# Kernel optimization log

Hardware: AMD Instinct MI355X
Metric: run time of the kernel (lower is better)

Reference implementation:

```python
import jax, jax.numpy as jnp
import numpy as np

LOG2 = np.float32(np.log(2.0))

def _jsd_pos(p):
    # get_positive_expectation, measure='JSD', average=False
    return LOG2 - jax.nn.softplus(-p)

def setup_inputs() -> dict:
    key = jax.random.key(0)
    k1, k2, k3, k4, k5, k6 = jax.random.split(key, 6)
    N, G, D = 65536, 512, 256
    batch_1 = jnp.sort(jax.random.randint(k1, (N,), 0, G))
    batch_2 = jnp.sort(jax.random.randint(k2, (N,), 0, G))
    z1 = jax.random.normal(k3, (N, D), dtype=jnp.float32)
    z2 = jax.random.normal(k4, (N, D), dtype=jnp.float32)
    g1 = jax.random.normal(k5, (G, D), dtype=jnp.float32)
    g2 = jax.random.normal(k6, (G, D), dtype=jnp.float32)
    return {"batch_1": batch_1, "batch_2": batch_2, "z1": z1, "z2": z2, "g1": g1, "g2": g2}

def reference(batch_1, batch_2, z1, z2, g1, g2):
    # pos_mask scatter-build -> dense one-hot [N, G]
    pos_mask_1 = jax.nn.one_hot(batch_1, g1.shape[0], dtype=z1.dtype)
    pos_mask_2 = jax.nn.one_hot(batch_2, g2.shape[0], dtype=z2.dtype)
    # masked node-graph similarity matrices [N, G]
    self_sim_1 = (z1 @ g1.T) * pos_mask_1
    self_sim_2 = (z2 @ g2.T) * pos_mask_2
    cross_sim_12 = (z1 @ g2.T) * pos_mask_1
    cross_sim_21 = (z2 @ g1.T) * pos_mask_2
    # sep=True branch: per-node row sums, L2 distance over nodes
    self_js_11 = _jsd_pos(self_sim_1).sum(1)
    cross_js_12 = _jsd_pos(cross_sim_12).sum(1)
    self_js_22 = _jsd_pos(self_sim_2).sum(1)
    cross_js_21 = _jsd_pos(cross_sim_21).sum(1)
    L_1 = jnp.sqrt(jnp.sum((self_js_11 - cross_js_12) ** 2))
    L_2 = jnp.sqrt(jnp.sum((self_js_22 - cross_js_21) ** 2))
    return L_1 + L_2
```

## Files before the change

### kernel.cpp

```cpp
#include <hip/hip_runtime.h>
#include <math.h>

__device__ __forceinline__ float spn(float p) {
    return fmaxf(-p, 0.0f) + __logf(1.0f + __expf(-fabsf(p)));
}

__device__ __forceinline__ float dot4(float4 a, float4 b) {
    return a.x * b.x + a.y * b.y + a.z * b.z + a.w * b.w;
}

__device__ __forceinline__ float wave64_reduce(float x) {
    int t;
    t = __builtin_amdgcn_update_dpp(0, __builtin_bit_cast(int, x), 0x111, 0xf, 0xf, true);
    x += __builtin_bit_cast(float, t);
    t = __builtin_amdgcn_update_dpp(0, __builtin_bit_cast(int, x), 0x112, 0xf, 0xf, true);
    x += __builtin_bit_cast(float, t);
    t = __builtin_amdgcn_update_dpp(0, __builtin_bit_cast(int, x), 0x114, 0xf, 0xf, true);
    x += __builtin_bit_cast(float, t);
    t = __builtin_amdgcn_update_dpp(0, __builtin_bit_cast(int, x), 0x118, 0xf, 0xf, true);
    x += __builtin_bit_cast(float, t);
    t = __builtin_amdgcn_update_dpp(0, __builtin_bit_cast(int, x), 0x142, 0xa, 0xf, true);
    x += __builtin_bit_cast(float, t);
    t = __builtin_amdgcn_update_dpp(0, __builtin_bit_cast(int, x), 0x143, 0xc, 0xf, true);
    x += __builtin_bit_cast(float, t);
    return x;
}

typedef const void __attribute__((address_space(1)))* gas_ptr;
typedef void       __attribute__((address_space(3)))* las_ptr;

__device__ __forceinline__ void stage_row(const float* grow, float* lrow, int lane) {
    __builtin_amdgcn_global_load_lds((gas_ptr)(grow + lane * 4), (las_ptr)lrow,
                                     16, 0, 0);
}

#define NBLOCKS 4096
#define NPB 16
#define NPW 4

__global__ __launch_bounds__(256) void jsd_dot_kernel(
    const int*   __restrict__ b1,
    const int*   __restrict__ b2,
    const float* __restrict__ z1,
    const float* __restrict__ z2,
    const float* __restrict__ g1,
    const float* __restrict__ g2,
    float*       __restrict__ partials)
{
    __shared__ float zs1[NPB * 256];
    __shared__ float zs2[NPB * 256];

    const int wave = threadIdx.x >> 6;
    const int lane = threadIdx.x & 63;

    const int sbase = __builtin_amdgcn_readfirstlane(blockIdx.x * NPB + wave * NPW);

    #pragma unroll
    for (int j = 0; j < NPW; ++j) {
        stage_row(z1 + (size_t)(sbase + j) * 256, &zs1[(wave * NPW + j) * 256], lane);
        stage_row(z2 + (size_t)(sbase + j) * 256, &zs2[(wave * NPW + j) * 256], lane);
    }

    int i1[NPW], i2[NPW];
    #pragma unroll
    for (int j = 0; j < NPW; ++j) {
        i1[j] = b1[sbase + j];
        i2[j] = b2[sbase + j];
    }

    __syncthreads();

    float acc1 = 0.0f, acc2 = 0.0f;

    #pragma unroll
    for (int j = 0; j < NPW; ++j) {
        const float4 a1 = ((const float4*)&zs1[(wave * NPW + j) * 256])[lane];
        const float4 a2 = ((const float4*)&zs2[(wave * NPW + j) * 256])[lane];

        const float4 v11 = ((const float4*)(g1 + (size_t)i1[j] * 256))[lane];
        const float4 v12 = ((const float4*)(g2 + (size_t)i1[j] * 256))[lane];
        const float4 v22 = ((const float4*)(g2 + (size_t)i2[j] * 256))[lane];
        const float4 v21 = ((const float4*)(g1 + (size_t)i2[j] * 256))[lane];

        float s11 = wave64_reduce(dot4(a1, v11));
        float c12 = wave64_reduce(dot4(a1, v12));
        float s22 = wave64_reduce(dot4(a2, v22));
        float c21 = wave64_reduce(dot4(a2, v21));

        if (lane == 63) {
            float d1 = spn(c12) - spn(s11);
            float d2 = spn(c21) - spn(s22);
            acc1 += d1 * d1;
            acc2 += d2 * d2;
        }
    }

    __shared__ float s1[4], s2[4];
    if (lane == 63) { s1[wave] = acc1; s2[wave] = acc2; }
    __syncthreads();

    if (threadIdx.x == 0) {
        partials[blockIdx.x * 2 + 0] = s1[0] + s1[1] + s1[2] + s1[3];
        partials[blockIdx.x * 2 + 1] = s2[0] + s2[1] + s2[2] + s2[3];
    }
}

__global__ __launch_bounds__(256) void jsd_reduce_kernel(
    const float* __restrict__ partials,
    float*       __restrict__ out)
{
    const int tid  = threadIdx.x;
    const int wave = tid >> 6;
    const int lane = tid & 63;

    float a = 0.0f, b = 0.0f;
    #pragma unroll
    for (int i = 0; i < NBLOCKS / 256; ++i) {
        a += partials[(i * 256 + tid) * 2 + 0];
        b += partials[(i * 256 + tid) * 2 + 1];
    }

    a = wave64_reduce(a);
    b = wave64_reduce(b);

    __shared__ float s1[4], s2[4];
    if (lane == 63) { s1[wave] = a; s2[wave] = b; }
    __syncthreads();

    if (tid == 0) {
        float t1 = s1[0] + s1[1] + s1[2] + s1[3];
        float t2 = s2[0] + s2[1] + s2[2] + s2[3];
        out[0] = sqrtf(t1) + sqrtf(t2);
    }
}

extern "C" void kernel_launch(void* const* d_in, const int* in_sizes, int n_in,
                              void* d_out, int out_size, void* d_ws, size_t ws_size,
                              hipStream_t stream) {
    const int*   b1 = (const int*)  d_in[0];
    const int*   b2 = (const int*)  d_in[1];
    const float* z1 = (const float*)d_in[2];
    const float* z2 = (const float*)d_in[3];
    const float* g1 = (const float*)d_in[4];
    const float* g2 = (const float*)d_in[5];
    float* out      = (float*)d_out;
    float* partials = (float*)d_ws;

    jsd_dot_kernel<<<NBLOCKS, 256, 0, stream>>>(b1, b2, z1, z2, g1, g2, partials);
    jsd_reduce_kernel<<<1, 256, 0, stream>>>(partials, out);
}
```

Baseline: 157.4 us.

## Double-buffer z row staging across node tiles in each block

```diff
diff --git a/kernel.cpp b/kernel.cpp
--- a/kernel.cpp
+++ b/kernel.cpp
@@ -34,9 +34,10 @@
                                      16, 0, 0);
 }
 
-#define NBLOCKS 4096
-#define NPB 16
-#define NPW 4
+#define NBLOCKS 2048
+#define NPB 32
+#define TPN 8
+#define NTILES 4
 
 __global__ __launch_bounds__(256) void jsd_dot_kernel(
     const int*   __restrict__ b1,
@@ -47,55 +48,62 @@
     const float* __restrict__ g2,
     float*       __restrict__ partials)
 {
-    __shared__ float zs1[NPB * 256];
-    __shared__ float zs2[NPB * 256];
+    __shared__ float zs[2][TPN][2][256];
+    __shared__ float s1[4], s2[4];
 
     const int wave = threadIdx.x >> 6;
     const int lane = threadIdx.x & 63;
+    const int bbase = __builtin_amdgcn_readfirstlane(blockIdx.x * NPB);
 
-    const int sbase = __builtin_amdgcn_readfirstlane(blockIdx.x * NPB + wave * NPW);
+    auto issue_tile = [&](int t, int buf) {
+        #pragma unroll
+        for (int r = wave * 4; r < wave * 4 + 4; ++r) {
+            const int n   = r >> 1;
+            const int arr = r & 1;
+            const float* src = (arr ? z2 : z1) + (size_t)(bbase + t * TPN + n) * 256;
+            stage_row(src, &zs[buf][n][arr][0], lane);
+        }
+    };
 
-    #pragma unroll
-    for (int j = 0; j < NPW; ++j) {
-        stage_row(z1 + (size_t)(sbase + j) * 256, &zs1[(wave * NPW + j) * 256], lane);
-        stage_row(z2 + (size_t)(sbase + j) * 256, &zs2[(wave * NPW + j) * 256], lane);
-    }
-
-    int i1[NPW], i2[NPW];
-    #pragma unroll
-    for (int j = 0; j < NPW; ++j) {
-        i1[j] = b1[sbase + j];
-        i2[j] = b2[sbase + j];
-    }
-
+    issue_tile(0, 0);
     __syncthreads();
 
     float acc1 = 0.0f, acc2 = 0.0f;
 
-    #pragma unroll
-    for (int j = 0; j < NPW; ++j) {
-        const float4 a1 = ((const float4*)&zs1[(wave * NPW + j) * 256])[lane];
-        const float4 a2 = ((const float4*)&zs2[(wave * NPW + j) * 256])[lane];
+    for (int t = 0; t < NTILES; ++t) {
+        if (t + 1 < NTILES) issue_tile(t + 1, (t + 1) & 1);
 
-        const float4 v11 = ((const float4*)(g1 + (size_t)i1[j] * 256))[lane];
-        const float4 v12 = ((const float4*)(g2 + (size_t)i1[j] * 256))[lane];
-        const float4 v22 = ((const float4*)(g2 + (size_t)i2[j] * 256))[lane];
-        const float4 v21 = ((const float4*)(g1 + (size_t)i2[j] * 256))[lane];
+        const int buf = t & 1;
+        #pragma unroll
+        for (int jj = 0; jj < 2; ++jj) {
+            const int n     = wave * 2 + jj;
+            const int gnode = bbase + t * TPN + n;
+            const int i1 = b1[gnode];
+            const int i2 = b2[gnode];
 
-        float s11 = wave64_reduce(dot4(a1, v11));
-        float c12 = wave64_reduce(dot4(a1, v12));
-        float s22 = wave64_reduce(dot4(a2, v22));
-        float c21 = wave64_reduce(dot4(a2, v21));
+            const float4 a1 = ((const float4*)&zs[buf][n][0][0])[lane];
+            const float4 a2 = ((const float4*)&zs[buf][n][1][0])[lane];
 
-        if (lane == 63) {
-            float d1 = spn(c12) - spn(s11);
-            float d2 = spn(c21) - spn(s22);
-            acc1 += d1 * d1;
-            acc2 += d2 * d2;
+            const float4 v11 = ((const float4*)(g1 + (size_t)i1 * 256))[lane];
+            const float4 v12 = ((const float4*)(g2 + (size_t)i1 * 256))[lane];
+            const float4 v22 = ((const float4*)(g2 + (size_t)i2 * 256))[lane];
+            const float4 v21 = ((const float4*)(g1 + (size_t)i2 * 256))[lane];
+
+            float s11 = wave64_reduce(dot4(a1, v11));
+            float c12 = wave64_reduce(dot4(a1, v12));
+            float s22 = wave64_reduce(dot4(a2, v22));
+            float c21 = wave64_reduce(dot4(a2, v21));
+
+            if (lane == 63) {
+                float d1 = spn(c12) - spn(s11);
+                float d2 = spn(c21) - spn(s22);
+                acc1 += d1 * d1;
+                acc2 += d2 * d2;
+            }
         }
+        __syncthreads();
     }
 
-    __shared__ float s1[4], s2[4];
     if (lane == 63) { s1[wave] = acc1; s2[wave] = acc2; }
     __syncthreads();
 
```

Result: no change. 160.2 us (+1.8%).
